# Optimization experiments

Hardware: AMD Instinct MI355X
Metric: run time of the kernel (lower is better)

## Reference

```python
import jax, jax.numpy as jnp
import numpy as np

T, B, A = 128, 512, 5
X, Y, Z, H, R = 2, 10, 32, 128, 128
LOG2PI = np.float32(np.log(2.0 * np.pi))


def setup_inputs() -> dict:
    key = jax.random.key(0)
    ks = iter(jax.random.split(key, 40))
    w = lambda *s: jax.random.normal(next(ks), s, jnp.float32) * 0.05
    return dict(
        states=jax.random.normal(next(ks), (T, B, Y), jnp.float32),
        eps=jax.random.normal(next(ks), (T - 1, B, A, Z), jnp.float32),
        enc_w1=w(A, X + Y + R, H), enc_b1=w(A, H),
        enc_w2=w(A, H, H), enc_b2=w(A, H),
        enc_mw=w(A, H, Z), enc_mb=w(A, Z),
        enc_sw=w(A, H, Z), enc_sb=w(A, Z),
        pri_w1=w(A, Y + R, H), pri_b1=w(A, H),
        pri_w2=w(A, H, H), pri_b2=w(A, H),
        pri_mw=w(A, H, Z), pri_mb=w(A, Z),
        pri_sw=w(A, H, Z), pri_sb=w(A, Z),
        dec_w1=w(A, Y + Z + R, H), dec_b1=w(A, H),
        dec_w2=w(A, H, H), dec_b2=w(A, H),
        dec_mw=w(A, H, X), dec_mb=w(A, X),
        dec_sw=w(A, H, X), dec_sb=w(A, X),
        gru_wih=w(A, X + Z, 3 * R), gru_whh=w(A, R, 3 * R),
        gru_bih=w(A, 3 * R), gru_bhh=w(A, 3 * R),
    )


def _lin(x, wt, b):
    # x: [B, A, I], wt: [A, I, O] -> [B, A, O]  (per-agent linear)
    return jnp.einsum('bai,aio->bao', x, wt) + b


def _mlp(x, w1, b1, w2, b2):
    return jax.nn.relu(_lin(jax.nn.relu(_lin(x, w1, b1)), w2, b2))


def reference(states, eps, enc_w1, enc_b1, enc_w2, enc_b2, enc_mw, enc_mb,
              enc_sw, enc_sb, pri_w1, pri_b1, pri_w2, pri_b2, pri_mw, pri_mb,
              pri_sw, pri_sb, dec_w1, dec_b1, dec_w2, dec_b2, dec_mw, dec_mb,
              dec_sw, dec_sb, gru_wih, gru_whh, gru_bih, gru_bhh):
    y_all = states[:-1]                              # [T-1, B, Y]
    x_all = states[1:].reshape(T - 1, B, A, X)       # per-agent next positions

    def step(carry, xs):
        h, kl, nll = carry                           # h: [B, A, R]
        y, x, e = xs                                 # y:[B,Y] x:[B,A,X] e:[B,A,Z]
        yb = jnp.broadcast_to(y[:, None, :], (B, A, Y))
        enc_h = _mlp(jnp.concatenate([x, yb, h], -1), enc_w1, enc_b1, enc_w2, enc_b2)
        enc_m = _lin(enc_h, enc_mw, enc_mb)
        enc_s = jax.nn.softplus(_lin(enc_h, enc_sw, enc_sb))
        pri_h = _mlp(jnp.concatenate([yb, h], -1), pri_w1, pri_b1, pri_w2, pri_b2)
        pri_m = _lin(pri_h, pri_mw, pri_mb)
        pri_s = jax.nn.softplus(_lin(pri_h, pri_sw, pri_sb))
        z = enc_m + enc_s * e                         # reparameterized sample
        dec_h = _mlp(jnp.concatenate([yb, z, h], -1), dec_w1, dec_b1, dec_w2, dec_b2)
        dec_m = _lin(dec_h, dec_mw, dec_mb)
        dec_s = jax.nn.softplus(_lin(dec_h, dec_sw, dec_sb))
        # GRU cell (torch gate order: r, z, n)
        gi = _lin(jnp.concatenate([x, z], -1), gru_wih, gru_bih)   # [B,A,3R]
        gh = _lin(h, gru_whh, gru_bhh)
        gir, giz, gin = jnp.split(gi, 3, -1)
        ghr, ghz, ghn = jnp.split(gh, 3, -1)
        r = jax.nn.sigmoid(gir + ghr)
        u = jax.nn.sigmoid(giz + ghz)
        n = jnp.tanh(gin + r * ghn)
        h_new = (1.0 - u) * n + u * h
        kl_t = 0.5 * jnp.sum(2.0 * jnp.log(pri_s) - 2.0 * jnp.log(enc_s)
                             + (enc_s ** 2 + (enc_m - pri_m) ** 2) / pri_s ** 2 - 1.0)
        nll_t = jnp.sum(0.5 * LOG2PI + jnp.log(dec_s) + 0.5 * ((x - dec_m) / dec_s) ** 2)
        return (h_new, kl + kl_t, nll + nll_t), None

    h0 = jnp.zeros((B, A, R), states.dtype)
    zero = jnp.zeros((), states.dtype)
    (h, kl, nll), _ = jax.lax.scan(step, (h0, zero, zero), (y_all, x_all, eps))
    return jnp.stack([kl, nll])  # [kl_loss, recon_loss]
```

## Files before the change

kernel.cpp:

```cpp
#include <hip/hip_runtime.h>

typedef __attribute__((ext_vector_type(8))) short bf16x8;
typedef __attribute__((ext_vector_type(4))) float f32x4;

#define MFMA_B16(A,B,C) __builtin_amdgcn_mfma_f32_16x16x32_bf16((A),(B),(C),0,0,0)

#define FO_ENC1 0
#define FO_PRI1 48
#define FO_DEC1 88
#define FO_GIH  136
#define FO_GHH  184
#define FO_ENC2 280
#define FO_PRI2 312
#define FO_DEC2 344
#define FO_MS   376
#define FO_DECMS 408
#define NFRAG   412

__device__ __forceinline__ unsigned short f2bf(float f) {
  union { float f; unsigned u; } v; v.f = f;
  unsigned r = (v.u + 0x7fffu + ((v.u >> 16) & 1u)) >> 16;
  return (unsigned short)r;
}
__device__ __forceinline__ float bf2f(unsigned short h) {
  union { unsigned u; float f; } v; v.u = ((unsigned)h) << 16;
  return v.f;
}
__device__ __forceinline__ float sigm_(float x) { return 1.f / (1.f + __expf(-x)); }
__device__ __forceinline__ float tanh_(float x) {
  x = fminf(fmaxf(x, -15.f), 15.f);
  float e = __expf(-2.f * x);
  return (1.f - e) / (1.f + e);
}
__device__ __forceinline__ float splus_(float x) {
  return fmaxf(x, 0.f) + log1pf(__expf(-fabsf(x)));
}

__global__ void prep_kernel(const float* __restrict__ ew1, const float* __restrict__ pw1,
                            const float* __restrict__ dw1, const float* __restrict__ wih,
                            const float* __restrict__ whh, const float* __restrict__ ew2,
                            const float* __restrict__ pw2, const float* __restrict__ dw2,
                            const float* __restrict__ emw, const float* __restrict__ esw,
                            const float* __restrict__ pmw, const float* __restrict__ psw,
                            const float* __restrict__ dmw, const float* __restrict__ dsw,
                            unsigned short* __restrict__ ws)
{
  int blk = blockIdx.x;
  int a = blk / NFRAG, f = blk % NFRAG;
  int l = threadIdx.x, lg = l >> 4, ln = l & 15;
  float v[8];

  if (f < FO_PRI1) {
    int fi = f, nt = fi / 6, kb = fi % 6, n = nt * 16 + ln;
#pragma unroll
    for (int j = 0; j < 8; ++j) {
      int mk = kb * 32 + lg * 8 + j;
      int r = (mk < 2) ? mk : (mk >= 34 && mk < 44) ? 2 + (mk - 34)
            : (mk >= 64) ? 12 + (mk - 64) : -1;
      v[j] = (r >= 0) ? ew1[((size_t)a * 140 + r) * 128 + n] : 0.f;
    }
  } else if (f < FO_DEC1) {
    int fi = f - FO_PRI1, nt = fi / 5, kb = 1 + fi % 5, n = nt * 16 + ln;
#pragma unroll
    for (int j = 0; j < 8; ++j) {
      int mk = kb * 32 + lg * 8 + j;
      int r = (mk >= 34 && mk < 44) ? (mk - 34) : (mk >= 64) ? 10 + (mk - 64) : -1;
      v[j] = (r >= 0) ? pw1[((size_t)a * 138 + r) * 128 + n] : 0.f;
    }
  } else if (f < FO_GIH) {
    int fi = f - FO_DEC1, nt = fi / 6, kb = fi % 6, n = nt * 16 + ln;
#pragma unroll
    for (int j = 0; j < 8; ++j) {
      int mk = kb * 32 + lg * 8 + j;
      int r = (mk >= 2 && mk < 34) ? 10 + (mk - 2) : (mk >= 34 && mk < 44) ? (mk - 34)
            : (mk >= 64) ? 42 + (mk - 64) : -1;
      v[j] = (r >= 0) ? dw1[((size_t)a * 170 + r) * 128 + n] : 0.f;
    }
  } else if (f < FO_GHH) {
    int fi = f - FO_GIH, nt = fi / 2, kb = fi % 2, n = nt * 16 + ln;
#pragma unroll
    for (int j = 0; j < 8; ++j) {
      int mk = kb * 32 + lg * 8 + j;
      v[j] = (mk < 34) ? wih[((size_t)a * 34 + mk) * 384 + n] : 0.f;
    }
  } else if (f < FO_ENC2) {
    int fi = f - FO_GHH, nt = fi / 4, kb = fi % 4, n = nt * 16 + ln;
#pragma unroll
    for (int j = 0; j < 8; ++j) {
      int r = kb * 32 + lg * 8 + j;
      v[j] = whh[((size_t)a * 128 + r) * 384 + n];
    }
  } else if (f < FO_DEC2) {
    int fi = f - FO_ENC2;
    const float* W = (fi < 32) ? ew2 : pw2;
    fi &= 31;
    int nt = fi / 4, kb = fi % 4, n = nt * 16 + ln;
#pragma unroll
    for (int j = 0; j < 8; ++j) {
      int r = kb * 32 + lg * 8 + j;
      v[j] = W[((size_t)a * 128 + r) * 128 + n];
    }
  } else if (f < FO_MS) {
    int fi = f - FO_DEC2, nt = fi / 4, kb = fi % 4, n = nt * 16 + ln;
#pragma unroll
    for (int j = 0; j < 8; ++j) {
      int r = kb * 32 + lg * 8 + j;
      v[j] = dw2[((size_t)a * 128 + r) * 128 + n];
    }
  } else if (f < FO_DECMS) {
    int fi = f - FO_MS, mat = fi / 8, rem = fi % 8, nt = rem / 4, kb = rem % 4;
    int n = nt * 16 + ln;
    const float* W = (mat == 0) ? emw : (mat == 1) ? esw : (mat == 2) ? pmw : psw;
#pragma unroll
    for (int j = 0; j < 8; ++j) {
      int r = kb * 32 + lg * 8 + j;
      v[j] = W[((size_t)a * 128 + r) * 32 + n];
    }
  } else {
    int kb = f - FO_DECMS;
#pragma unroll
    for (int j = 0; j < 8; ++j) {
      int r = kb * 32 + lg * 8 + j;
      v[j] = (ln < 2) ? dmw[((size_t)a * 128 + r) * 2 + ln]
           : (ln < 4) ? dsw[((size_t)a * 128 + r) * 2 + (ln - 2)] : 0.f;
    }
  }
  unsigned short* dst = ws + (size_t)blk * 512 + l * 8;
#pragma unroll
  for (int j = 0; j < 8; ++j) dst[j] = f2bf(v[j]);
}

__global__ __launch_bounds__(512, 2) void vrnn_main(
    const float* __restrict__ states, const float* __restrict__ eps,
    const float* __restrict__ eb1, const float* __restrict__ eb2,
    const float* __restrict__ emb, const float* __restrict__ esb,
    const float* __restrict__ pb1, const float* __restrict__ pb2,
    const float* __restrict__ pmb, const float* __restrict__ psb,
    const float* __restrict__ db1, const float* __restrict__ db2,
    const float* __restrict__ dmb, const float* __restrict__ dsb,
    const float* __restrict__ bih, const float* __restrict__ bhh,
    const unsigned short* __restrict__ frags, float* __restrict__ out)
{
  const int a = blockIdx.y;
  const int b0 = blockIdx.x * 16;
  const int tid = threadIdx.x;
  const int w = tid >> 6, l = tid & 63, lg = l >> 4, ln = l & 15;

  __shared__ __align__(16) unsigned short ghh_lds[96 * 512];
  __shared__ __align__(16) unsigned short ms_lds[32 * 512];
  __shared__ __align__(16) unsigned short dms_lds[4 * 512];
  __shared__ __align__(16) unsigned short master[16 * 200];
  __shared__ __align__(16) unsigned short t1e[16 * 136], t1p[16 * 136];
  __shared__ __align__(16) unsigned short he[16 * 136], hp[16 * 136];
  __shared__ float msbuf[2][16][32];
  __shared__ float red[16];

  const unsigned short* fa = frags + (size_t)a * NFRAG * 512;

  {
    const uint4* s1 = (const uint4*)(fa + (size_t)FO_GHH * 512);
    uint4* d1 = (uint4*)ghh_lds;
    for (int i = tid; i < 96 * 64; i += 512) d1[i] = s1[i];
    const uint4* s2 = (const uint4*)(fa + (size_t)FO_MS * 512);
    uint4* d2 = (uint4*)ms_lds;
    for (int i = tid; i < 32 * 64; i += 512) d2[i] = s2[i];
    const uint4* s3 = (const uint4*)(fa + (size_t)FO_DECMS * 512);
    uint4* d3 = (uint4*)dms_lds;
    if (tid < 256) d3[tid] = s3[tid];
  }
  for (int i = tid; i < 16 * 200; i += 512) master[i] = 0;

  bf16x8 be1[6], bp1[5], be2[4], bp2[4], bd2[4], bD[12];
#pragma unroll
  for (int kb = 0; kb < 6; ++kb)
    be1[kb] = *(const bf16x8*)(fa + (size_t)(FO_ENC1 + w * 6 + kb) * 512 + l * 8);
#pragma unroll
  for (int kb = 0; kb < 5; ++kb)
    bp1[kb] = *(const bf16x8*)(fa + (size_t)(FO_PRI1 + w * 5 + kb) * 512 + l * 8);
#pragma unroll
  for (int kb = 0; kb < 4; ++kb) {
    be2[kb] = *(const bf16x8*)(fa + (size_t)(FO_ENC2 + w * 4 + kb) * 512 + l * 8);
    bp2[kb] = *(const bf16x8*)(fa + (size_t)(FO_PRI2 + w * 4 + kb) * 512 + l * 8);
    bd2[kb] = *(const bf16x8*)(fa + (size_t)(FO_DEC2 + w * 4 + kb) * 512 + l * 8);
  }
  if (w < 4) {
#pragma unroll
    for (int j = 0; j < 2; ++j)
#pragma unroll
      for (int kb = 0; kb < 6; ++kb)
        bD[j * 6 + kb] = *(const bf16x8*)(fa + (size_t)(FO_DEC1 + (w + 4 * j) * 6 + kb) * 512 + l * 8);
  } else {
    int kx = w - 4;
#pragma unroll
    for (int g = 0; g < 3; ++g)
#pragma unroll
      for (int j = 0; j < 2; ++j)
#pragma unroll
        for (int kb = 0; kb < 2; ++kb)
          bD[g * 4 + j * 2 + kb] =
            *(const bf16x8*)(fa + (size_t)(FO_GIH + (g * 8 + kx + 4 * j) * 2 + kb) * 512 + l * 8);
  }

  float eb1v = eb1[a * 128 + w * 16 + ln], pb1v = pb1[a * 128 + w * 16 + ln];
  float eb2v = eb2[a * 128 + w * 16 + ln], pb2v = pb2[a * 128 + w * 16 + ln];
  float db2v = db2[a * 128 + w * 16 + ln];
  float hbm = 0.f, hbs = 0.f, d1b0 = 0.f, d1b1 = 0.f, dmsb = 0.f;
  float ghb[6] = {0.f, 0.f, 0.f, 0.f, 0.f, 0.f};
  if (w < 2) { hbm = emb[a * 32 + w * 16 + ln]; hbs = esb[a * 32 + w * 16 + ln]; }
  else if (w < 4) { hbm = pmb[a * 32 + (w - 2) * 16 + ln]; hbs = psb[a * 32 + (w - 2) * 16 + ln]; }
  if (w < 4) { d1b0 = db1[a * 128 + w * 16 + ln]; d1b1 = db1[a * 128 + (w + 4) * 16 + ln]; }
  else {
    int kx = w - 4;
#pragma unroll
    for (int g = 0; g < 3; ++g)
#pragma unroll
      for (int j = 0; j < 2; ++j)
        ghb[g * 2 + j] = bih[a * 384 + g * 128 + (kx + 4 * j) * 16 + ln]
                       + bhh[a * 384 + g * 128 + (kx + 4 * j) * 16 + ln];
  }
  if (w == 0) dmsb = (ln < 2) ? dmb[a * 2 + ln] : (ln < 4) ? dsb[a * 2 + (ln - 2)] : 0.f;

  __syncthreads();

  if (tid < 160) {
    int row = tid / 10, c = tid - row * 10;
    master[row * 200 + 34 + c] = f2bf(states[(size_t)b0 * 10 + tid]);
  }
  if (tid >= 192 && tid < 224) {
    int i = tid - 192, row = i >> 1, c = i & 1;
    master[row * 200 + c] = f2bf(states[((size_t)512 + b0 + row) * 10 + a * 2 + c]);
  }
  float e_cur[4] = {0.f, 0.f, 0.f, 0.f};
  if (w < 2) {
#pragma unroll
    for (int q = 0; q < 4; ++q)
      e_cur[q] = eps[((size_t)(b0 + 4 * lg + q) * 5 + a) * 32 + w * 16 + ln];
  }
  float xv[4] = {0.f, 0.f, 0.f, 0.f};
  float kl = 0.f, nll = 0.f;
  f32x4 em = {0, 0, 0, 0}, esv = {0, 0, 0, 0};
  f32x4 gh[3][2];
  float hn[8];
  __syncthreads();

  for (int t = 0; t < 127; ++t) {
    if (w == 0 && t > 0) {
      f32x4 acc = {dmsb, dmsb, dmsb, dmsb};
#pragma unroll
      for (int kb = 0; kb < 4; ++kb) {
        bf16x8 ad = *(const bf16x8*)&he[ln * 136 + kb * 32 + lg * 8];
        bf16x8 bf = *(const bf16x8*)&dms_lds[kb * 512 + l * 8];
        acc = MFMA_B16(ad, bf, acc);
      }
#pragma unroll
      for (int q = 0; q < 4; ++q) {
        float sv = __shfl(splus_(acc[q]), l + 2);
        if (ln < 2) {
          float d = (xv[q] - acc[q]) / sv;
          nll += 0.9189385332f + __logf(sv) + 0.5f * d * d;
        }
      }
    }
    {
      bf16x8 am[6];
#pragma unroll
      for (int kb = 0; kb < 6; ++kb)
        am[kb] = *(const bf16x8*)&master[ln * 200 + kb * 32 + lg * 8];
      f32x4 a1 = {eb1v, eb1v, eb1v, eb1v}, a2 = {pb1v, pb1v, pb1v, pb1v};
#pragma unroll
      for (int kb = 0; kb < 6; ++kb) a1 = MFMA_B16(am[kb], be1[kb], a1);
#pragma unroll
      for (int kb = 0; kb < 5; ++kb) a2 = MFMA_B16(am[kb + 1], bp1[kb], a2);
#pragma unroll
      for (int q = 0; q < 4; ++q) {
        t1e[(4 * lg + q) * 136 + w * 16 + ln] = f2bf(fmaxf(a1[q], 0.f));
        t1p[(4 * lg + q) * 136 + w * 16 + ln] = f2bf(fmaxf(a2[q], 0.f));
      }
    }
    __syncthreads();

    {
      bf16x8 ae[4], ap[4];
#pragma unroll
      for (int kb = 0; kb < 4; ++kb) {
        ae[kb] = *(const bf16x8*)&t1e[ln * 136 + kb * 32 + lg * 8];
        ap[kb] = *(const bf16x8*)&t1p[ln * 136 + kb * 32 + lg * 8];
      }
      f32x4 a1 = {eb2v, eb2v, eb2v, eb2v}, a2 = {pb2v, pb2v, pb2v, pb2v};
#pragma unroll
      for (int kb = 0; kb < 4; ++kb) {
        a1 = MFMA_B16(ae[kb], be2[kb], a1);
        a2 = MFMA_B16(ap[kb], bp2[kb], a2);
      }
#pragma unroll
      for (int q = 0; q < 4; ++q) {
        he[(4 * lg + q) * 136 + w * 16 + ln] = f2bf(fmaxf(a1[q], 0.f));
        hp[(4 * lg + q) * 136 + w * 16 + ln] = f2bf(fmaxf(a2[q], 0.f));
      }
    }
    __syncthreads();

    {
      float e_nxt[4] = {0.f, 0.f, 0.f, 0.f};
      if (w < 2 && t < 126) {
#pragma unroll
        for (int q = 0; q < 4; ++q)
          e_nxt[q] = eps[((size_t)((t + 1) * 512 + b0 + 4 * lg + q) * 5 + a) * 32 + w * 16 + ln];
      }
      if (w < 4) {
        const unsigned short* hsrc = (w < 2) ? he : hp;
        bf16x8 ah[4];
#pragma unroll
        for (int kb = 0; kb < 4; ++kb)
          ah[kb] = *(const bf16x8*)&hsrc[ln * 136 + kb * 32 + lg * 8];
        int mbase = ((w < 2) ? 0 : 16) + (w & 1) * 4;
        f32x4 m = {hbm, hbm, hbm, hbm}, s = {hbs, hbs, hbs, hbs};
#pragma unroll
        for (int kb = 0; kb < 4; ++kb) {
          m = MFMA_B16(ah[kb], *(const bf16x8*)&ms_lds[(mbase + kb) * 512 + l * 8], m);
          s = MFMA_B16(ah[kb], *(const bf16x8*)&ms_lds[(mbase + 8 + kb) * 512 + l * 8], s);
        }
        if (w < 2) {
          em = m;
#pragma unroll
          for (int q = 0; q < 4; ++q) {
            esv[q] = splus_(s[q]);
            master[(4 * lg + q) * 200 + 2 + w * 16 + ln] = f2bf(m[q] + esv[q] * e_cur[q]);
          }
        } else {
#pragma unroll
          for (int q = 0; q < 4; ++q) {
            msbuf[0][4 * lg + q][(w - 2) * 16 + ln] = m[q];
            msbuf[1][4 * lg + q][(w - 2) * 16 + ln] = splus_(s[q]);
          }
        }
      } else {
        int kx = w - 4;
        bf16x8 ahh[4];
#pragma unroll
        for (int kb = 0; kb < 4; ++kb)
          ahh[kb] = *(const bf16x8*)&master[ln * 200 + (kb + 2) * 32 + lg * 8];
#pragma unroll
        for (int g = 0; g < 3; ++g)
#pragma unroll
          for (int j = 0; j < 2; ++j) {
            float bv = ghb[g * 2 + j];
            gh[g][j] = (f32x4){bv, bv, bv, bv};
          }
#pragma unroll
        for (int kb = 0; kb < 4; ++kb)
#pragma unroll
          for (int g = 0; g < 3; ++g)
#pragma unroll
            for (int j = 0; j < 2; ++j)
              gh[g][j] = MFMA_B16(ahh[kb],
                *(const bf16x8*)&ghh_lds[(size_t)((g * 8 + kx + 4 * j) * 4 + kb) * 512 + l * 8],
                gh[g][j]);
      }
      if (w < 2 && t < 126) {
#pragma unroll
        for (int q = 0; q < 4; ++q) e_cur[q] = e_nxt[q];
      }
    }
    __syncthreads();

    if (w == 0) {
#pragma unroll
      for (int q = 0; q < 4; ++q)
        xv[q] = states[((size_t)(t + 1) * 512 + b0 + 4 * lg + q) * 10 + a * 2 + (ln & 1)];
    }
    if (w < 4) {
      bf16x8 amn[6];
#pragma unroll
      for (int kb = 0; kb < 6; ++kb)
        amn[kb] = *(const bf16x8*)&master[ln * 200 + kb * 32 + lg * 8];
#pragma unroll
      for (int j = 0; j < 2; ++j) {
        float bv = (j == 0) ? d1b0 : d1b1;
        f32x4 acc = {bv, bv, bv, bv};
#pragma unroll
        for (int kb = 0; kb < 6; ++kb) acc = MFMA_B16(amn[kb], bD[j * 6 + kb], acc);
#pragma unroll
        for (int q = 0; q < 4; ++q)
          t1e[(4 * lg + q) * 136 + (w + 4 * j) * 16 + ln] = f2bf(fmaxf(acc[q], 0.f));
      }
      if (w < 2) {
#pragma unroll
        for (int q = 0; q < 4; ++q) {
          float pm = msbuf[0][4 * lg + q][w * 16 + ln];
          float ps = msbuf[1][4 * lg + q][w * 16 + ln];
          float dm = em[q] - pm;
          float es2 = esv[q] * esv[q];
          kl += 0.5f * (2.f * __logf(ps) - 2.f * __logf(esv[q]) + (es2 + dm * dm) / (ps * ps) - 1.f);
        }
      }
    } else {
      int kx = w - 4;
      bf16x8 am2[2];
#pragma unroll
      for (int kb = 0; kb < 2; ++kb)
        am2[kb] = *(const bf16x8*)&master[ln * 200 + kb * 32 + lg * 8];
      f32x4 gi[3][2];
#pragma unroll
      for (int g = 0; g < 3; ++g)
#pragma unroll
        for (int j = 0; j < 2; ++j) gi[g][j] = (f32x4){0.f, 0.f, 0.f, 0.f};
#pragma unroll
      for (int kb = 0; kb < 2; ++kb)
#pragma unroll
        for (int g = 0; g < 3; ++g)
#pragma unroll
          for (int j = 0; j < 2; ++j)
            gi[g][j] = MFMA_B16(am2[kb], bD[g * 4 + j * 2 + kb], gi[g][j]);
#pragma unroll
      for (int j = 0; j < 2; ++j)
#pragma unroll
        for (int q = 0; q < 4; ++q) {
          float r_ = sigm_(gi[0][j][q] + gh[0][j][q]);
          float u_ = sigm_(gi[1][j][q] + gh[1][j][q]);
          float n_ = tanh_(gi[2][j][q] + r_ * gh[2][j][q]);
          float ho = bf2f(master[(4 * lg + q) * 200 + 64 + (kx + 4 * j) * 16 + ln]);
          hn[j * 4 + q] = (1.f - u_) * n_ + u_ * ho;
        }
    }
    __syncthreads();

    {
      bf16x8 ad[4];
#pragma unroll
      for (int kb = 0; kb < 4; ++kb)
        ad[kb] = *(const bf16x8*)&t1e[ln * 136 + kb * 32 + lg * 8];
      f32x4 acc = {db2v, db2v, db2v, db2v};
#pragma unroll
      for (int kb = 0; kb < 4; ++kb) acc = MFMA_B16(ad[kb], bd2[kb], acc);
#pragma unroll
      for (int q = 0; q < 4; ++q)
        he[(4 * lg + q) * 136 + w * 16 + ln] = f2bf(fmaxf(acc[q], 0.f));
    }
    if (w >= 4) {
      int kx = w - 4;
#pragma unroll
      for (int j = 0; j < 2; ++j)
#pragma unroll
        for (int q = 0; q < 4; ++q)
          master[(4 * lg + q) * 200 + 64 + (kx + 4 * j) * 16 + ln] = f2bf(hn[j * 4 + q]);
    }
    if (t < 126) {
      if (w >= 1 && w <= 3) {
        int i = (w - 1) * 64 + l;
        if (i < 160) {
          int row = i / 10, c = i - row * 10;
          master[row * 200 + 34 + c] = f2bf(states[((size_t)(t + 1) * 512 + b0) * 10 + i]);
        }
      }
      if (w == 0 && l < 32) {
        int row = l >> 1, c = l & 1;
        master[row * 200 + c] = f2bf(states[((size_t)(t + 2) * 512 + b0 + row) * 10 + a * 2 + c]);
      }
    }
    __syncthreads();
  }

  if (w == 0) {
    f32x4 acc = {dmsb, dmsb, dmsb, dmsb};
#pragma unroll
    for (int kb = 0; kb < 4; ++kb) {
      bf16x8 ad = *(const bf16x8*)&he[ln * 136 + kb * 32 + lg * 8];
      bf16x8 bf = *(const bf16x8*)&dms_lds[kb * 512 + l * 8];
      acc = MFMA_B16(ad, bf, acc);
    }
#pragma unroll
    for (int q = 0; q < 4; ++q) {
      float sv = __shfl(splus_(acc[q]), l + 2);
      if (ln < 2) {
        float d = (xv[q] - acc[q]) / sv;
        nll += 0.9189385332f + __logf(sv) + 0.5f * d * d;
      }
    }
  }

#pragma unroll
  for (int off = 32; off > 0; off >>= 1) {
    kl += __shfl_down(kl, off);
    nll += __shfl_down(nll, off);
  }
  if (l == 0) { red[w] = kl; red[8 + w] = nll; }
  __syncthreads();
  if (tid == 0) {
    float K = 0.f, N = 0.f;
#pragma unroll
    for (int i = 0; i < 8; ++i) { K += red[i]; N += red[8 + i]; }
    atomicAdd(out, K);
    atomicAdd(out + 1, N);
  }
}

extern "C" void kernel_launch(void* const* d_in, const int* in_sizes, int n_in,
                              void* d_out, int out_size, void* d_ws, size_t ws_size,
                              hipStream_t stream) {
  (void)in_sizes; (void)n_in; (void)out_size; (void)ws_size;
  const float* states = (const float*)d_in[0];
  const float* eps    = (const float*)d_in[1];
  const float* ew1 = (const float*)d_in[2];
  const float* eb1 = (const float*)d_in[3];
  const float* ew2 = (const float*)d_in[4];
  const float* eb2 = (const float*)d_in[5];
  const float* emw = (const float*)d_in[6];
  const float* emb = (const float*)d_in[7];
  const float* esw = (const float*)d_in[8];
  const float* esb = (const float*)d_in[9];
  const float* pw1 = (const float*)d_in[10];
  const float* pb1 = (const float*)d_in[11];
  const float* pw2 = (const float*)d_in[12];
  const float* pb2 = (const float*)d_in[13];
  const float* pmw = (const float*)d_in[14];
  const float* pmb = (const float*)d_in[15];
  const float* psw = (const float*)d_in[16];
  const float* psb = (const float*)d_in[17];
  const float* dw1 = (const float*)d_in[18];
  const float* db1 = (const float*)d_in[19];
  const float* dw2 = (const float*)d_in[20];
  const float* db2 = (const float*)d_in[21];
  const float* dmw = (const float*)d_in[22];
  const float* dmb = (const float*)d_in[23];
  const float* dsw = (const float*)d_in[24];
  const float* dsb = (const float*)d_in[25];
  const float* wih = (const float*)d_in[26];
  const float* whh = (const float*)d_in[27];
  const float* bih = (const float*)d_in[28];
  const float* bhh = (const float*)d_in[29];

  unsigned short* frags = (unsigned short*)d_ws;
  float* out = (float*)d_out;

  hipMemsetAsync(d_out, 0, 2 * sizeof(float), stream);
  prep_kernel<<<dim3(5 * NFRAG), dim3(64), 0, stream>>>(
      ew1, pw1, dw1, wih, whh, ew2, pw2, dw2, emw, esw, pmw, psw, dmw, dsw, frags);
  vrnn_main<<<dim3(32, 5), dim3(512), 0, stream>>>(
      states, eps, eb1, eb2, emb, esb, pb1, pb2, pmb, psb,
      db1, db2, dmb, dsb, bih, bhh, frags, out);
}
```

Baseline: 1.099 ms.

## Process 32 batch rows per block with 1024 threads and stream weight fragments

Each block now covers 32 batch rows using 16 waves, two groups of 8 waves sharing one LDS copy of the GRU hidden weights. The grid drops from 160 to 80 blocks. Weight fragments are no longer held in registers for the whole loop; each step reloads them from global memory (relying on cache), and the mean/std weights move from LDS to global loads. This is meant to halve the per-block LDS weight staging and relieve register pressure, at the cost of repeated global or L2 loads on every serial step and fewer blocks to spread across CUs.

```diff
diff --git a/kernel.cpp b/kernel.cpp
--- a/kernel.cpp
+++ b/kernel.cpp
@@ -16,6 +16,9 @@
 #define FO_MS   376
 #define FO_DECMS 408
 #define NFRAG   412
+
+#define MS 200
+#define TS 136
 
 __device__ __forceinline__ unsigned short f2bf(float f) {
   union { float f; unsigned u; } v; v.f = f;
@@ -130,7 +133,9 @@
   for (int j = 0; j < 8; ++j) dst[j] = f2bf(v[j]);
 }
 
-__global__ __launch_bounds__(512, 2) void vrnn_main(
+#define LD_FRAG(idx) (*(const bf16x8*)(fa + (size_t)(idx) * 512 + l * 8))
+
+__global__ __launch_bounds__(1024, 1) void vrnn_main(
     const float* __restrict__ states, const float* __restrict__ eps,
     const float* __restrict__ eb1, const float* __restrict__ eb2,
     const float* __restrict__ emb, const float* __restrict__ esb,
@@ -142,75 +147,41 @@
     const unsigned short* __restrict__ frags, float* __restrict__ out)
 {
   const int a = blockIdx.y;
-  const int b0 = blockIdx.x * 16;
+  const int b0 = blockIdx.x * 32;
   const int tid = threadIdx.x;
   const int w = tid >> 6, l = tid & 63, lg = l >> 4, ln = l & 15;
+  const int wl = w & 7, rg = w >> 3, R = rg * 16;
 
   __shared__ __align__(16) unsigned short ghh_lds[96 * 512];
-  __shared__ __align__(16) unsigned short ms_lds[32 * 512];
   __shared__ __align__(16) unsigned short dms_lds[4 * 512];
-  __shared__ __align__(16) unsigned short master[16 * 200];
-  __shared__ __align__(16) unsigned short t1e[16 * 136], t1p[16 * 136];
-  __shared__ __align__(16) unsigned short he[16 * 136], hp[16 * 136];
-  __shared__ float msbuf[2][16][32];
-  __shared__ float red[16];
+  __shared__ __align__(16) unsigned short master[32 * MS];
+  __shared__ __align__(16) unsigned short t1e[32 * TS], t1p[32 * TS];
+  __shared__ __align__(16) unsigned short he[32 * TS], hp[32 * TS];
+  __shared__ float msbuf[2][32][32];
+  __shared__ float red[32];
 
   const unsigned short* fa = frags + (size_t)a * NFRAG * 512;
 
   {
     const uint4* s1 = (const uint4*)(fa + (size_t)FO_GHH * 512);
     uint4* d1 = (uint4*)ghh_lds;
-    for (int i = tid; i < 96 * 64; i += 512) d1[i] = s1[i];
-    const uint4* s2 = (const uint4*)(fa + (size_t)FO_MS * 512);
-    uint4* d2 = (uint4*)ms_lds;
-    for (int i = tid; i < 32 * 64; i += 512) d2[i] = s2[i];
+    for (int i = tid; i < 96 * 64; i += 1024) d1[i] = s1[i];
     const uint4* s3 = (const uint4*)(fa + (size_t)FO_DECMS * 512);
     uint4* d3 = (uint4*)dms_lds;
     if (tid < 256) d3[tid] = s3[tid];
   }
-  for (int i = tid; i < 16 * 200; i += 512) master[i] = 0;
-
-  bf16x8 be1[6], bp1[5], be2[4], bp2[4], bd2[4], bD[12];
-#pragma unroll
-  for (int kb = 0; kb < 6; ++kb)
-    be1[kb] = *(const bf16x8*)(fa + (size_t)(FO_ENC1 + w * 6 + kb) * 512 + l * 8);
-#pragma unroll
-  for (int kb = 0; kb < 5; ++kb)
-    bp1[kb] = *(const bf16x8*)(fa + (size_t)(FO_PRI1 + w * 5 + kb) * 512 + l * 8);
-#pragma unroll
-  for (int kb = 0; kb < 4; ++kb) {
-    be2[kb] = *(const bf16x8*)(fa + (size_t)(FO_ENC2 + w * 4 + kb) * 512 + l * 8);
-    bp2[kb] = *(const bf16x8*)(fa + (size_t)(FO_PRI2 + w * 4 + kb) * 512 + l * 8);
-    bd2[kb] = *(const bf16x8*)(fa + (size_t)(FO_DEC2 + w * 4 + kb) * 512 + l * 8);
-  }
-  if (w < 4) {
-#pragma unroll
-    for (int j = 0; j < 2; ++j)
-#pragma unroll
-      for (int kb = 0; kb < 6; ++kb)
-        bD[j * 6 + kb] = *(const bf16x8*)(fa + (size_t)(FO_DEC1 + (w + 4 * j) * 6 + kb) * 512 + l * 8);
-  } else {
-    int kx = w - 4;
-#pragma unroll
-    for (int g = 0; g < 3; ++g)
-#pragma unroll
-      for (int j = 0; j < 2; ++j)
-#pragma unroll
-        for (int kb = 0; kb < 2; ++kb)
-          bD[g * 4 + j * 2 + kb] =
-            *(const bf16x8*)(fa + (size_t)(FO_GIH + (g * 8 + kx + 4 * j) * 2 + kb) * 512 + l * 8);
-  }
-
-  float eb1v = eb1[a * 128 + w * 16 + ln], pb1v = pb1[a * 128 + w * 16 + ln];
-  float eb2v = eb2[a * 128 + w * 16 + ln], pb2v = pb2[a * 128 + w * 16 + ln];
-  float db2v = db2[a * 128 + w * 16 + ln];
+  for (int i = tid; i < 32 * MS; i += 1024) master[i] = 0;
+
+  float eb1v = eb1[a * 128 + wl * 16 + ln], pb1v = pb1[a * 128 + wl * 16 + ln];
+  float eb2v = eb2[a * 128 + wl * 16 + ln], pb2v = pb2[a * 128 + wl * 16 + ln];
+  float db2v = db2[a * 128 + wl * 16 + ln];
   float hbm = 0.f, hbs = 0.f, d1b0 = 0.f, d1b1 = 0.f, dmsb = 0.f;
   float ghb[6] = {0.f, 0.f, 0.f, 0.f, 0.f, 0.f};
-  if (w < 2) { hbm = emb[a * 32 + w * 16 + ln]; hbs = esb[a * 32 + w * 16 + ln]; }
-  else if (w < 4) { hbm = pmb[a * 32 + (w - 2) * 16 + ln]; hbs = psb[a * 32 + (w - 2) * 16 + ln]; }
-  if (w < 4) { d1b0 = db1[a * 128 + w * 16 + ln]; d1b1 = db1[a * 128 + (w + 4) * 16 + ln]; }
+  if (wl < 2) { hbm = emb[a * 32 + wl * 16 + ln]; hbs = esb[a * 32 + wl * 16 + ln]; }
+  else if (wl < 4) { hbm = pmb[a * 32 + (wl - 2) * 16 + ln]; hbs = psb[a * 32 + (wl - 2) * 16 + ln]; }
+  if (wl < 4) { d1b0 = db1[a * 128 + wl * 16 + ln]; d1b1 = db1[a * 128 + (wl + 4) * 16 + ln]; }
   else {
-    int kx = w - 4;
+    int kx = wl - 4;
 #pragma unroll
     for (int g = 0; g < 3; ++g)
 #pragma unroll
@@ -218,23 +189,23 @@
         ghb[g * 2 + j] = bih[a * 384 + g * 128 + (kx + 4 * j) * 16 + ln]
                        + bhh[a * 384 + g * 128 + (kx + 4 * j) * 16 + ln];
   }
-  if (w == 0) dmsb = (ln < 2) ? dmb[a * 2 + ln] : (ln < 4) ? dsb[a * 2 + (ln - 2)] : 0.f;
+  if (wl == 0) dmsb = (ln < 2) ? dmb[a * 2 + ln] : (ln < 4) ? dsb[a * 2 + (ln - 2)] : 0.f;
 
   __syncthreads();
 
-  if (tid < 160) {
+  if (tid < 320) {
     int row = tid / 10, c = tid - row * 10;
-    master[row * 200 + 34 + c] = f2bf(states[(size_t)b0 * 10 + tid]);
-  }
-  if (tid >= 192 && tid < 224) {
-    int i = tid - 192, row = i >> 1, c = i & 1;
-    master[row * 200 + c] = f2bf(states[((size_t)512 + b0 + row) * 10 + a * 2 + c]);
+    master[row * MS + 34 + c] = f2bf(states[((size_t)b0 + row) * 10 + c]);
+  }
+  if (tid >= 384 && tid < 448) {
+    int i = tid - 384, row = i >> 1, c = i & 1;
+    master[row * MS + c] = f2bf(states[((size_t)512 + b0 + row) * 10 + a * 2 + c]);
   }
   float e_cur[4] = {0.f, 0.f, 0.f, 0.f};
-  if (w < 2) {
+  if (wl < 2) {
 #pragma unroll
     for (int q = 0; q < 4; ++q)
-      e_cur[q] = eps[((size_t)(b0 + 4 * lg + q) * 5 + a) * 32 + w * 16 + ln];
+      e_cur[q] = eps[((size_t)(b0 + R + 4 * lg + q) * 5 + a) * 32 + wl * 16 + ln];
   }
   float xv[4] = {0.f, 0.f, 0.f, 0.f};
   float kl = 0.f, nll = 0.f;
@@ -244,11 +215,11 @@
   __syncthreads();
 
   for (int t = 0; t < 127; ++t) {
-    if (w == 0 && t > 0) {
+    if (wl == 0 && t > 0) {
       f32x4 acc = {dmsb, dmsb, dmsb, dmsb};
 #pragma unroll
       for (int kb = 0; kb < 4; ++kb) {
-        bf16x8 ad = *(const bf16x8*)&he[ln * 136 + kb * 32 + lg * 8];
+        bf16x8 ad = *(const bf16x8*)&he[(R + ln) * TS + kb * 32 + lg * 8];
         bf16x8 bf = *(const bf16x8*)&dms_lds[kb * 512 + l * 8];
         acc = MFMA_B16(ad, bf, acc);
       }
@@ -262,144 +233,168 @@
       }
     }
     {
+      bf16x8 f1[6], f2[5];
+#pragma unroll
+      for (int kb = 0; kb < 6; ++kb) f1[kb] = LD_FRAG(FO_ENC1 + wl * 6 + kb);
+#pragma unroll
+      for (int kb = 0; kb < 5; ++kb) f2[kb] = LD_FRAG(FO_PRI1 + wl * 5 + kb);
       bf16x8 am[6];
 #pragma unroll
       for (int kb = 0; kb < 6; ++kb)
-        am[kb] = *(const bf16x8*)&master[ln * 200 + kb * 32 + lg * 8];
+        am[kb] = *(const bf16x8*)&master[(R + ln) * MS + kb * 32 + lg * 8];
       f32x4 a1 = {eb1v, eb1v, eb1v, eb1v}, a2 = {pb1v, pb1v, pb1v, pb1v};
 #pragma unroll
-      for (int kb = 0; kb < 6; ++kb) a1 = MFMA_B16(am[kb], be1[kb], a1);
-#pragma unroll
-      for (int kb = 0; kb < 5; ++kb) a2 = MFMA_B16(am[kb + 1], bp1[kb], a2);
+      for (int kb = 0; kb < 6; ++kb) a1 = MFMA_B16(am[kb], f1[kb], a1);
+#pragma unroll
+      for (int kb = 0; kb < 5; ++kb) a2 = MFMA_B16(am[kb + 1], f2[kb], a2);
 #pragma unroll
       for (int q = 0; q < 4; ++q) {
-        t1e[(4 * lg + q) * 136 + w * 16 + ln] = f2bf(fmaxf(a1[q], 0.f));
-        t1p[(4 * lg + q) * 136 + w * 16 + ln] = f2bf(fmaxf(a2[q], 0.f));
+        t1e[(R + 4 * lg + q) * TS + wl * 16 + ln] = f2bf(fmaxf(a1[q], 0.f));
+        t1p[(R + 4 * lg + q) * TS + wl * 16 + ln] = f2bf(fmaxf(a2[q], 0.f));
       }
     }
     __syncthreads();
 
     {
+      bf16x8 g1[4], g2[4];
+#pragma unroll
+      for (int kb = 0; kb < 4; ++kb) {
+        g1[kb] = LD_FRAG(FO_ENC2 + wl * 4 + kb);
+        g2[kb] = LD_FRAG(FO_PRI2 + wl * 4 + kb);
+      }
       bf16x8 ae[4], ap[4];
 #pragma unroll
       for (int kb = 0; kb < 4; ++kb) {
-        ae[kb] = *(const bf16x8*)&t1e[ln * 136 + kb * 32 + lg * 8];
-        ap[kb] = *(const bf16x8*)&t1p[ln * 136 + kb * 32 + lg * 8];
+        ae[kb] = *(const bf16x8*)&t1e[(R + ln) * TS + kb * 32 + lg * 8];
+        ap[kb] = *(const bf16x8*)&t1p[(R + ln) * TS + kb * 32 + lg * 8];
       }
       f32x4 a1 = {eb2v, eb2v, eb2v, eb2v}, a2 = {pb2v, pb2v, pb2v, pb2v};
 #pragma unroll
       for (int kb = 0; kb < 4; ++kb) {
-        a1 = MFMA_B16(ae[kb], be2[kb], a1);
-        a2 = MFMA_B16(ap[kb], bp2[kb], a2);
+        a1 = MFMA_B16(ae[kb], g1[kb], a1);
+        a2 = MFMA_B16(ap[kb], g2[kb], a2);
       }
 #pragma unroll
       for (int q = 0; q < 4; ++q) {
-        he[(4 * lg + q) * 136 + w * 16 + ln] = f2bf(fmaxf(a1[q], 0.f));
-        hp[(4 * lg + q) * 136 + w * 16 + ln] = f2bf(fmaxf(a2[q], 0.f));
+        he[(R + 4 * lg + q) * TS + wl * 16 + ln] = f2bf(fmaxf(a1[q], 0.f));
+        hp[(R + 4 * lg + q) * TS + wl * 16 + ln] = f2bf(fmaxf(a2[q], 0.f));
       }
     }
     __syncthreads();
 
-    {
-      float e_nxt[4] = {0.f, 0.f, 0.f, 0.f};
-      if (w < 2 && t < 126) {
-#pragma unroll
-        for (int q = 0; q < 4; ++q)
-          e_nxt[q] = eps[((size_t)((t + 1) * 512 + b0 + 4 * lg + q) * 5 + a) * 32 + w * 16 + ln];
-      }
-      if (w < 4) {
-        const unsigned short* hsrc = (w < 2) ? he : hp;
-        bf16x8 ah[4];
-#pragma unroll
-        for (int kb = 0; kb < 4; ++kb)
-          ah[kb] = *(const bf16x8*)&hsrc[ln * 136 + kb * 32 + lg * 8];
-        int mbase = ((w < 2) ? 0 : 16) + (w & 1) * 4;
-        f32x4 m = {hbm, hbm, hbm, hbm}, s = {hbs, hbs, hbs, hbs};
-#pragma unroll
-        for (int kb = 0; kb < 4; ++kb) {
-          m = MFMA_B16(ah[kb], *(const bf16x8*)&ms_lds[(mbase + kb) * 512 + l * 8], m);
-          s = MFMA_B16(ah[kb], *(const bf16x8*)&ms_lds[(mbase + 8 + kb) * 512 + l * 8], s);
-        }
-        if (w < 2) {
-          em = m;
-#pragma unroll
-          for (int q = 0; q < 4; ++q) {
-            esv[q] = splus_(s[q]);
-            master[(4 * lg + q) * 200 + 2 + w * 16 + ln] = f2bf(m[q] + esv[q] * e_cur[q]);
-          }
-        } else {
-#pragma unroll
-          for (int q = 0; q < 4; ++q) {
-            msbuf[0][4 * lg + q][(w - 2) * 16 + ln] = m[q];
-            msbuf[1][4 * lg + q][(w - 2) * 16 + ln] = splus_(s[q]);
-          }
+    if (wl < 4) {
+      const unsigned short* hs = (wl < 2) ? he : hp;
+      int fbase = FO_MS + ((wl < 2) ? 0 : 16) + (wl & 1) * 4;
+      bf16x8 fm[4], fs[4];
+#pragma unroll
+      for (int kb = 0; kb < 4; ++kb) {
+        fm[kb] = LD_FRAG(fbase + kb);
+        fs[kb] = LD_FRAG(fbase + 8 + kb);
+      }
+      bf16x8 ah[4];
+#pragma unroll
+      for (int kb = 0; kb < 4; ++kb)
+        ah[kb] = *(const bf16x8*)&hs[(R + ln) * TS + kb * 32 + lg * 8];
+      f32x4 m = {hbm, hbm, hbm, hbm}, s = {hbs, hbs, hbs, hbs};
+#pragma unroll
+      for (int kb = 0; kb < 4; ++kb) {
+        m = MFMA_B16(ah[kb], fm[kb], m);
+        s = MFMA_B16(ah[kb], fs[kb], s);
+      }
+      if (wl < 2) {
+        em = m;
+#pragma unroll
+        for (int q = 0; q < 4; ++q) {
+          esv[q] = splus_(s[q]);
+          master[(R + 4 * lg + q) * MS + 2 + wl * 16 + ln] = f2bf(m[q] + esv[q] * e_cur[q]);
         }
       } else {
-        int kx = w - 4;
-        bf16x8 ahh[4];
-#pragma unroll
-        for (int kb = 0; kb < 4; ++kb)
-          ahh[kb] = *(const bf16x8*)&master[ln * 200 + (kb + 2) * 32 + lg * 8];
+#pragma unroll
+        for (int q = 0; q < 4; ++q) {
+          msbuf[0][R + 4 * lg + q][(wl - 2) * 16 + ln] = m[q];
+          msbuf[1][R + 4 * lg + q][(wl - 2) * 16 + ln] = splus_(s[q]);
+        }
+      }
+    } else {
+      int kx = wl - 4;
+      bf16x8 ahh[4];
+#pragma unroll
+      for (int kb = 0; kb < 4; ++kb)
+        ahh[kb] = *(const bf16x8*)&master[(R + ln) * MS + (kb + 2) * 32 + lg * 8];
+#pragma unroll
+      for (int g = 0; g < 3; ++g)
+#pragma unroll
+        for (int j = 0; j < 2; ++j) {
+          float bv = ghb[g * 2 + j];
+          gh[g][j] = (f32x4){bv, bv, bv, bv};
+        }
+#pragma unroll
+      for (int kb = 0; kb < 4; ++kb)
 #pragma unroll
         for (int g = 0; g < 3; ++g)
 #pragma unroll
-          for (int j = 0; j < 2; ++j) {
-            float bv = ghb[g * 2 + j];
-            gh[g][j] = (f32x4){bv, bv, bv, bv};
-          }
-#pragma unroll
-        for (int kb = 0; kb < 4; ++kb)
-#pragma unroll
-          for (int g = 0; g < 3; ++g)
-#pragma unroll
-            for (int j = 0; j < 2; ++j)
-              gh[g][j] = MFMA_B16(ahh[kb],
-                *(const bf16x8*)&ghh_lds[(size_t)((g * 8 + kx + 4 * j) * 4 + kb) * 512 + l * 8],
-                gh[g][j]);
-      }
-      if (w < 2 && t < 126) {
-#pragma unroll
-        for (int q = 0; q < 4; ++q) e_cur[q] = e_nxt[q];
-      }
+          for (int j = 0; j < 2; ++j)
+            gh[g][j] = MFMA_B16(ahh[kb],
+              *(const bf16x8*)&ghh_lds[(size_t)((g * 8 + kx + 4 * j) * 4 + kb) * 512 + l * 8],
+              gh[g][j]);
     }
     __syncthreads();
 
-    if (w == 0) {
+    if (wl < 2 && t < 126) {
 #pragma unroll
       for (int q = 0; q < 4; ++q)
-        xv[q] = states[((size_t)(t + 1) * 512 + b0 + 4 * lg + q) * 10 + a * 2 + (ln & 1)];
-    }
-    if (w < 4) {
+        e_cur[q] = eps[((size_t)((t + 1) * 512 + b0 + R + 4 * lg + q) * 5 + a) * 32 + wl * 16 + ln];
+    }
+    if (wl == 0) {
+#pragma unroll
+      for (int q = 0; q < 4; ++q)
+        xv[q] = states[((size_t)(t + 1) * 512 + b0 + R + 4 * lg + q) * 10 + a * 2 + (ln & 1)];
+    }
+    if (wl < 4) {
+      bf16x8 fd[12];
+#pragma unroll
+      for (int j = 0; j < 2; ++j)
+#pragma unroll
+        for (int kb = 0; kb < 6; ++kb)
+          fd[j * 6 + kb] = LD_FRAG(FO_DEC1 + (wl + 4 * j) * 6 + kb);
       bf16x8 amn[6];
 #pragma unroll
       for (int kb = 0; kb < 6; ++kb)
-        amn[kb] = *(const bf16x8*)&master[ln * 200 + kb * 32 + lg * 8];
+        amn[kb] = *(const bf16x8*)&master[(R + ln) * MS + kb * 32 + lg * 8];
 #pragma unroll
       for (int j = 0; j < 2; ++j) {
         float bv = (j == 0) ? d1b0 : d1b1;
         f32x4 acc = {bv, bv, bv, bv};
 #pragma unroll
-        for (int kb = 0; kb < 6; ++kb) acc = MFMA_B16(amn[kb], bD[j * 6 + kb], acc);
+        for (int kb = 0; kb < 6; ++kb) acc = MFMA_B16(amn[kb], fd[j * 6 + kb], acc);
 #pragma unroll
         for (int q = 0; q < 4; ++q)
-          t1e[(4 * lg + q) * 136 + (w + 4 * j) * 16 + ln] = f2bf(fmaxf(acc[q], 0.f));
-      }
-      if (w < 2) {
+          t1e[(R + 4 * lg + q) * TS + (wl + 4 * j) * 16 + ln] = f2bf(fmaxf(acc[q], 0.f));
+      }
+      if (wl < 2) {
 #pragma unroll
         for (int q = 0; q < 4; ++q) {
-          float pm = msbuf[0][4 * lg + q][w * 16 + ln];
-          float ps = msbuf[1][4 * lg + q][w * 16 + ln];
+          float pm = msbuf[0][R + 4 * lg + q][wl * 16 + ln];
+          float ps = msbuf[1][R + 4 * lg + q][wl * 16 + ln];
           float dm = em[q] - pm;
           float es2 = esv[q] * esv[q];
           kl += 0.5f * (2.f * __logf(ps) - 2.f * __logf(esv[q]) + (es2 + dm * dm) / (ps * ps) - 1.f);
         }
       }
     } else {
-      int kx = w - 4;
+      int kx = wl - 4;
+      bf16x8 fg[12];
+#pragma unroll
+      for (int g = 0; g < 3; ++g)
+#pragma unroll
+        for (int j = 0; j < 2; ++j)
+#pragma unroll
+          for (int kb = 0; kb < 2; ++kb)
+            fg[g * 4 + j * 2 + kb] = LD_FRAG(FO_GIH + (g * 8 + kx + 4 * j) * 2 + kb);
       bf16x8 am2[2];
 #pragma unroll
       for (int kb = 0; kb < 2; ++kb)
-        am2[kb] = *(const bf16x8*)&master[ln * 200 + kb * 32 + lg * 8];
+        am2[kb] = *(const bf16x8*)&master[(R + ln) * MS + kb * 32 + lg * 8];
       f32x4 gi[3][2];
 #pragma unroll
       for (int g = 0; g < 3; ++g)
@@ -411,7 +406,7 @@
         for (int g = 0; g < 3; ++g)
 #pragma unroll
           for (int j = 0; j < 2; ++j)
-            gi[g][j] = MFMA_B16(am2[kb], bD[g * 4 + j * 2 + kb], gi[g][j]);
+            gi[g][j] = MFMA_B16(am2[kb], fg[g * 4 + j * 2 + kb], gi[g][j]);
 #pragma unroll
       for (int j = 0; j < 2; ++j)
 #pragma unroll
@@ -419,53 +414,54 @@
           float r_ = sigm_(gi[0][j][q] + gh[0][j][q]);
           float u_ = sigm_(gi[1][j][q] + gh[1][j][q]);
           float n_ = tanh_(gi[2][j][q] + r_ * gh[2][j][q]);
-          float ho = bf2f(master[(4 * lg + q) * 200 + 64 + (kx + 4 * j) * 16 + ln]);
+          float ho = bf2f(master[(R + 4 * lg + q) * MS + 64 + (kx + 4 * j) * 16 + ln]);
           hn[j * 4 + q] = (1.f - u_) * n_ + u_ * ho;
         }
     }
     __syncthreads();
 
     {
+      bf16x8 fd2[4];
+#pragma unroll
+      for (int kb = 0; kb < 4; ++kb) fd2[kb] = LD_FRAG(FO_DEC2 + wl * 4 + kb);
       bf16x8 ad[4];
 #pragma unroll
       for (int kb = 0; kb < 4; ++kb)
-        ad[kb] = *(const bf16x8*)&t1e[ln * 136 + kb * 32 + lg * 8];
+        ad[kb] = *(const bf16x8*)&t1e[(R + ln) * TS + kb * 32 + lg * 8];
       f32x4 acc = {db2v, db2v, db2v, db2v};
 #pragma unroll
-      for (int kb = 0; kb < 4; ++kb) acc = MFMA_B16(ad[kb], bd2[kb], acc);
+      for (int kb = 0; kb < 4; ++kb) acc = MFMA_B16(ad[kb], fd2[kb], acc);
 #pragma unroll
       for (int q = 0; q < 4; ++q)
-        he[(4 * lg + q) * 136 + w * 16 + ln] = f2bf(fmaxf(acc[q], 0.f));
-    }
-    if (w >= 4) {
-      int kx = w - 4;
+        he[(R + 4 * lg + q) * TS + wl * 16 + ln] = f2bf(fmaxf(acc[q], 0.f));
+    }
+    if (wl >= 4) {
+      int kx = wl - 4;
 #pragma unroll
       for (int j = 0; j < 2; ++j)
 #pragma unroll
         for (int q = 0; q < 4; ++q)
-          master[(4 * lg + q) * 200 + 64 + (kx + 4 * j) * 16 + ln] = f2bf(hn[j * 4 + q]);
+          master[(R + 4 * lg + q) * MS + 64 + (kx + 4 * j) * 16 + ln] = f2bf(hn[j * 4 + q]);
     }
     if (t < 126) {
-      if (w >= 1 && w <= 3) {
+      if (w >= 1 && w <= 5) {
         int i = (w - 1) * 64 + l;
-        if (i < 160) {
-          int row = i / 10, c = i - row * 10;
-          master[row * 200 + 34 + c] = f2bf(states[((size_t)(t + 1) * 512 + b0) * 10 + i]);
-        }
-      }
-      if (w == 0 && l < 32) {
+        int row = i / 10, c = i - row * 10;
+        master[row * MS + 34 + c] = f2bf(states[((size_t)(t + 1) * 512 + b0 + row) * 10 + c]);
+      }
+      if (w == 6) {
         int row = l >> 1, c = l & 1;
-        master[row * 200 + c] = f2bf(states[((size_t)(t + 2) * 512 + b0 + row) * 10 + a * 2 + c]);
+        master[row * MS + c] = f2bf(states[((size_t)(t + 2) * 512 + b0 + row) * 10 + a * 2 + c]);
       }
     }
     __syncthreads();
   }
 
-  if (w == 0) {
+  if (wl == 0) {
     f32x4 acc = {dmsb, dmsb, dmsb, dmsb};
 #pragma unroll
     for (int kb = 0; kb < 4; ++kb) {
-      bf16x8 ad = *(const bf16x8*)&he[ln * 136 + kb * 32 + lg * 8];
+      bf16x8 ad = *(const bf16x8*)&he[(R + ln) * TS + kb * 32 + lg * 8];
       bf16x8 bf = *(const bf16x8*)&dms_lds[kb * 512 + l * 8];
       acc = MFMA_B16(ad, bf, acc);
     }
@@ -484,12 +480,12 @@
     kl += __shfl_down(kl, off);
     nll += __shfl_down(nll, off);
   }
-  if (l == 0) { red[w] = kl; red[8 + w] = nll; }
+  if (l == 0) { red[w] = kl; red[16 + w] = nll; }
   __syncthreads();
   if (tid == 0) {
     float K = 0.f, N = 0.f;
 #pragma unroll
-    for (int i = 0; i < 8; ++i) { K += red[i]; N += red[8 + i]; }
+    for (int i = 0; i < 16; ++i) { K += red[i]; N += red[16 + i]; }
     atomicAdd(out, K);
     atomicAdd(out + 1, N);
   }
@@ -536,7 +532,7 @@
   hipMemsetAsync(d_out, 0, 2 * sizeof(float), stream);
   prep_kernel<<<dim3(5 * NFRAG), dim3(64), 0, stream>>>(
       ew1, pw1, dw1, wih, whh, ew2, pw2, dw2, emw, esw, pmw, psw, dmw, dsw, frags);
-  vrnn_main<<<dim3(32, 5), dim3(512), 0, stream>>>(
+  vrnn_main<<<dim3(16, 5), dim3(1024), 0, stream>>>(
       states, eps, eb1, eb2, emb, esb, pb1, pb2, pmb, psb,
       db1, db2, dmb, dsb, bih, bhh, frags, out);
 }
```

Measured after the change: 3.946 ms. 259% more time.
